# Kernel optimization log

Measured on AMD Instinct MI355X. Metric: run time of the kernel, lower is better.

Reference implementation:

```python
import math
import jax, jax.numpy as jnp
import numpy as np

N, L, D, H = 2, 2048, 1024, 16
DK = D // H  # 64


def setup_inputs() -> dict:
    key = jax.random.key(0)
    k1, k2, k3, k4, k5 = jax.random.split(key, 5)
    scale = 1.0 / math.sqrt(D)
    return {
        "values": jax.random.normal(k1, (N, L, D), dtype=jnp.float32),
        "keys": jax.random.normal(k2, (N, L, D), dtype=jnp.float32),
        "queries": jax.random.normal(k3, (N, L, D), dtype=jnp.float32),
        "fc_out_w": jax.random.normal(k4, (D, D), dtype=jnp.float32) * scale,
        "fc_out_b": jax.random.normal(k5, (D,), dtype=jnp.float32) * scale,
    }


def reference(values, keys, queries, fc_out_w, fc_out_b):
    n, q_len, _ = queries.shape
    k_len = keys.shape[1]
    v = values.reshape(n, k_len, H, DK)
    k = keys.reshape(n, k_len, H, DK)
    q = queries.reshape(n, q_len, H, DK)
    # NOTE: the original module never applies its per-head Linear layers (dead code),
    # and scales logits AFTER the QK einsum.
    energy = jnp.einsum('nqhd,nkhd->nhqk', q, k)  # [N,H,q,k]
    p_attn = jax.nn.softmax(energy / math.sqrt(DK), axis=3)
    attn = jnp.einsum('nhqk,nkhd->nqhd', p_attn, v).reshape(n, q_len, H * DK)
    # fc_out: torch Linear -> x @ W.T + b
    return attn @ fc_out_w.T + fc_out_b
```

## Files before the change

kernel.cpp:

```cpp
#include <hip/hip_runtime.h>
#include <hip/hip_bf16.h>

#define NBATCH 2
#define SEQ    2048
#define DMODEL 1024
#define NHEAD  16
#define DHEAD  64
#define NHTOT  (NBATCH*NHEAD)

typedef __attribute__((ext_vector_type(8)))  short          short8;
typedef __attribute__((ext_vector_type(4)))  float          f32x4;
typedef __attribute__((ext_vector_type(16))) float          f32x16;
typedef __attribute__((ext_vector_type(4)))  unsigned short ushort4v;

__device__ __forceinline__ unsigned short f2bf(float x) {
  union { __hip_bfloat16 b; unsigned short u; } c;
  c.b = __float2bfloat16(x);
  return c.u;
}

__device__ __forceinline__ unsigned int cvt_pk_bf16(float lo, float hi) {
  unsigned int r;
  asm("v_cvt_pk_bf16_f32 %0, %1, %2" : "=v"(r) : "v"(lo), "v"(hi));
  return r;
}

__device__ __forceinline__ void gl_lds16(const unsigned short* g, unsigned short* l) {
  __builtin_amdgcn_global_load_lds(
      (const __attribute__((address_space(1))) void*)g,
      (__attribute__((address_space(3))) void*)l, 16, 0, 0);
}

__global__ __launch_bounds__(256) void cvt_qk(const float* __restrict__ q,
                                              const float* __restrict__ k,
                                              unsigned short* __restrict__ qb,
                                              unsigned short* __restrict__ kb) {
  const float QSCALE = 0.125f * 1.44269504088896340736f;
  int e = (blockIdx.x * 256 + threadIdx.x) * 8;
  int n = e >> 21;
  int r = e & ((1 << 21) - 1);
  int l = r >> 10;
  int c = r & 1023;
  int h = c >> 6;
  int d = c & 63;
  size_t dst = ((size_t)(n * NHEAD + h) * SEQ + l) * DHEAD + d;
  float4 q0 = *reinterpret_cast<const float4*>(q + e);
  float4 q1 = *reinterpret_cast<const float4*>(q + e + 4);
  float4 k0 = *reinterpret_cast<const float4*>(k + e);
  float4 k1 = *reinterpret_cast<const float4*>(k + e + 4);
  union { unsigned short u[8]; short8 s; } qo, ko;
  qo.u[0]=f2bf(q0.x*QSCALE); qo.u[1]=f2bf(q0.y*QSCALE);
  qo.u[2]=f2bf(q0.z*QSCALE); qo.u[3]=f2bf(q0.w*QSCALE);
  qo.u[4]=f2bf(q1.x*QSCALE); qo.u[5]=f2bf(q1.y*QSCALE);
  qo.u[6]=f2bf(q1.z*QSCALE); qo.u[7]=f2bf(q1.w*QSCALE);
  ko.u[0]=f2bf(k0.x); ko.u[1]=f2bf(k0.y); ko.u[2]=f2bf(k0.z); ko.u[3]=f2bf(k0.w);
  ko.u[4]=f2bf(k1.x); ko.u[5]=f2bf(k1.y); ko.u[6]=f2bf(k1.z); ko.u[7]=f2bf(k1.w);
  *reinterpret_cast<short8*>(qb + dst) = qo.s;
  *reinterpret_cast<short8*>(kb + dst) = ko.s;
}

__global__ __launch_bounds__(256) void vtrans(const float* __restrict__ v,
                                              unsigned short* __restrict__ vt) {
  __shared__ __align__(16) unsigned short t[64][76];
  int bid = blockIdx.x;
  int nh = bid >> 5;
  int lt = bid & 31;
  int n = nh >> 4, h = nh & 15;
  int lbase = lt * 64;
  #pragma unroll
  for (int p = 0; p < 4; ++p) {
    int idx = p * 256 + threadIdx.x;
    int e = idx * 4;
    int l = e >> 6, d = e & 63;
    float4 x = *reinterpret_cast<const float4*>(
        v + ((size_t)n * SEQ + lbase + l) * DMODEL + h * DHEAD + d);
    ushort4v o;
    o.x = f2bf(x.x); o.y = f2bf(x.y); o.z = f2bf(x.z); o.w = f2bf(x.w);
    *reinterpret_cast<ushort4v*>(&t[l][d]) = o;
  }
  __syncthreads();
  #pragma unroll
  for (int p = 0; p < 4; ++p) {
    int idx = p * 256 + threadIdx.x;
    int d = idx >> 4, lq = (idx & 15) * 4;
    ushort4v o;
    o.x = t[lq + 0][d]; o.y = t[lq + 1][d];
    o.z = t[lq + 2][d]; o.w = t[lq + 3][d];
    *reinterpret_cast<ushort4v*>(
        vt + ((size_t)nh * DHEAD + d) * SEQ + lbase + lq) = o;
  }
}

__global__ __launch_bounds__(256) void cvt_w(const float* __restrict__ w,
                                             unsigned short* __restrict__ wb) {
  int e = (blockIdx.x * 256 + threadIdx.x) * 8;
  float4 w0 = *reinterpret_cast<const float4*>(w + e);
  float4 w1 = *reinterpret_cast<const float4*>(w + e + 4);
  union { unsigned short u[8]; short8 s; } wo;
  wo.u[0]=f2bf(w0.x); wo.u[1]=f2bf(w0.y); wo.u[2]=f2bf(w0.z); wo.u[3]=f2bf(w0.w);
  wo.u[4]=f2bf(w1.x); wo.u[5]=f2bf(w1.y); wo.u[6]=f2bf(w1.z); wo.u[7]=f2bf(w1.w);
  *reinterpret_cast<short8*>(wb + e) = wo.s;
}

__global__ __launch_bounds__(256, 2) void attn_fwd(const unsigned short* __restrict__ Qb,
                                                   const unsigned short* __restrict__ Kb,
                                                   const unsigned short* __restrict__ Vt,
                                                   unsigned short* __restrict__ Ab) {
  __shared__ __align__(16) unsigned short smem[4 * 4096];

  const int bid = blockIdx.x;
  const int nh = (bid & 7) * 4 + (bid >> 7);
  const int qt = (bid >> 3) & 15;
  const int tid  = threadIdx.x;
  const int wave = tid >> 6;
  const int lane = tid & 63;
  const int l31  = lane & 31;
  const int hi   = lane >> 5;

  const unsigned short* Kb_nh = Kb + (size_t)nh * SEQ * DHEAD;
  const unsigned short* Vt_nh = Vt + (size_t)nh * DHEAD * SEQ;

  const int qglob = qt * 128 + wave * 32 + l31;

  short8 bq[4];
  {
    const unsigned short* Qrow = Qb + ((size_t)nh * SEQ + qglob) * DHEAD + hi * 8;
    #pragma unroll
    for (int ds = 0; ds < 4; ++ds)
      bq[ds] = *reinterpret_cast<const short8*>(Qrow + ds * 16);
  }

  float m_run = -1e30f, l_run = 0.f;
  f32x16 acc[2];
  #pragma unroll
  for (int dt = 0; dt < 2; ++dt)
    #pragma unroll
    for (int r = 0; r < 16; ++r) acc[dt][r] = 0.f;

  int4 kreg[2], vreg[2];
  auto stage_load = [&](int kk) {
    #pragma unroll
    for (int j = 0; j < 2; ++j) {
      int c = j * 256 + tid;
      int row = c >> 3, cs = c & 7;
      kreg[j] = *reinterpret_cast<const int4*>(Kb_nh + (size_t)(kk + row) * DHEAD + cs * 8);
      vreg[j] = *reinterpret_cast<const int4*>(Vt_nh + (size_t)row * SEQ + kk + cs * 8);
    }
  };
  auto stage_write = [&](int buf) {
    unsigned short* kd = smem + buf * 4096;
    unsigned short* vd = smem + 2 * 4096 + buf * 4096;
    #pragma unroll
    for (int j = 0; j < 2; ++j) {
      int c = j * 256 + tid;
      int row = c >> 3, cs = c & 7;
      int dc = cs ^ (row & 7);
      *reinterpret_cast<int4*>(kd + (row * 8 + dc) * 8) = kreg[j];
      *reinterpret_cast<int4*>(vd + (row * 8 + dc) * 8) = vreg[j];
    }
  };

  stage_load(0);
  stage_write(0);
  __syncthreads();

  const int NT = SEQ / 64;
  for (int it = 0; it < NT; ++it) {
    const int cur = it & 1;
    const bool pf = (it + 1 < NT);
    if (pf) stage_load((it + 1) * 64);

    const unsigned short* kb = smem + cur * 4096;
    const unsigned short* vb = smem + 2 * 4096 + cur * 4096;

    f32x16 s[2];
    __builtin_amdgcn_s_setprio(1);
    #pragma unroll
    for (int kt = 0; kt < 2; ++kt) {
      #pragma unroll
      for (int r = 0; r < 16; ++r) s[kt][r] = 0.f;
      const int row = kt * 32 + l31;
      const int sw  = row & 7;
      const unsigned short* kr = kb + row * 64;
      #pragma unroll
      for (int ds = 0; ds < 4; ++ds) {
        short8 ak = *reinterpret_cast<const short8*>(kr + (((ds * 2 + hi) ^ sw) * 8));
        s[kt] = __builtin_amdgcn_mfma_f32_32x32x16_bf16(ak, bq[ds], s[kt], 0, 0, 0);
      }
    }
    __builtin_amdgcn_s_setprio(0);

    float pmax = s[0][0];
    #pragma unroll
    for (int kt = 0; kt < 2; ++kt)
      #pragma unroll
      for (int r = 0; r < 16; ++r) pmax = fmaxf(pmax, s[kt][r]);
    pmax = fmaxf(pmax, __shfl_xor(pmax, 32));

    if (!__all(pmax - m_run <= 8.0f)) {
      float mnew = fmaxf(m_run, pmax);
      float corr = exp2f(m_run - mnew);
      l_run *= corr;
      #pragma unroll
      for (int dt = 0; dt < 2; ++dt)
        #pragma unroll
        for (int r = 0; r < 16; ++r) acc[dt][r] *= corr;
      m_run = mnew;
    }

    float sum = 0.f;
    #pragma unroll
    for (int kt = 0; kt < 2; ++kt)
      #pragma unroll
      for (int r = 0; r < 16; ++r) {
        float p = exp2f(s[kt][r] - m_run);
        s[kt][r] = p;
        sum += p;
      }
    sum += __shfl_xor(sum, 32);
    l_run += sum;

    unsigned int pk[2][8];
    #pragma unroll
    for (int kt = 0; kt < 2; ++kt)
      #pragma unroll
      for (int i = 0; i < 8; ++i)
        pk[kt][i] = cvt_pk_bf16(s[kt][2 * i], s[kt][2 * i + 1]);

    unsigned int pa[4][4];
    #pragma unroll
    for (int ks = 0; ks < 4; ++ks) {
      const int t = ks >> 1, b = (ks & 1) * 4;
      pa[ks][0] = pk[t][b + 0]; pa[ks][2] = pk[t][b + 2];
      asm("v_permlane32_swap_b32 %0, %1" : "+v"(pa[ks][0]), "+v"(pa[ks][2]));
      pa[ks][1] = pk[t][b + 1]; pa[ks][3] = pk[t][b + 3];
      asm("v_permlane32_swap_b32 %0, %1" : "+v"(pa[ks][1]), "+v"(pa[ks][3]));
    }

    if (pf) stage_write(cur ^ 1);

    __builtin_amdgcn_s_setprio(1);
    #pragma unroll
    for (int dt = 0; dt < 2; ++dt) {
      const int row = dt * 32 + l31;
      const int sw  = row & 7;
      const unsigned short* vr = vb + row * 64;
      #pragma unroll
      for (int ks = 0; ks < 4; ++ks) {
        short8 av = *reinterpret_cast<const short8*>(vr + (((ks * 2 + hi) ^ sw) * 8));
        union { unsigned int u[4]; short8 s8; } pu;
        pu.u[0] = pa[ks][0]; pu.u[1] = pa[ks][1];
        pu.u[2] = pa[ks][2]; pu.u[3] = pa[ks][3];
        acc[dt] = __builtin_amdgcn_mfma_f32_32x32x16_bf16(av, pu.s8, acc[dt], 0, 0, 0);
      }
    }
    __builtin_amdgcn_s_setprio(0);
    __syncthreads();
  }

  unsigned short (*obuf)[32][76] = (unsigned short(*)[32][76])(&smem[0]);
  const float inv = 1.0f / l_run;
  const int n = nh >> 4, h = nh & 15;
  #pragma unroll
  for (int dt = 0; dt < 2; ++dt)
    #pragma unroll
    for (int q4 = 0; q4 < 4; ++q4) {
      ushort4v pv;
      pv.x = f2bf(acc[dt][q4 * 4 + 0] * inv);
      pv.y = f2bf(acc[dt][q4 * 4 + 1] * inv);
      pv.z = f2bf(acc[dt][q4 * 4 + 2] * inv);
      pv.w = f2bf(acc[dt][q4 * 4 + 3] * inv);
      *reinterpret_cast<ushort4v*>(&obuf[wave][l31][dt * 32 + q4 * 8 + hi * 4]) = pv;
    }
  __syncthreads();
  #pragma unroll
  for (int rep = 0; rep < 4; ++rep) {
    int idx = rep * 256 + tid;
    int qi = idx >> 3, ch = idx & 7;
    int w = qi >> 5, qr = qi & 31;
    union { unsigned short u[8]; short8 s; } vv;
    #pragma unroll
    for (int i = 0; i < 8; ++i) vv.u[i] = obuf[w][qr][ch * 8 + i];
    size_t orow = (size_t)n * SEQ + qt * 128 + qi;
    *reinterpret_cast<short8*>(Ab + orow * DMODEL + h * 64 + ch * 8) = vv.s;
  }
}

__global__ __launch_bounds__(256, 4) void fc_gemm(const unsigned short* __restrict__ Ab,
                                                  const unsigned short* __restrict__ Wb,
                                                  const float* __restrict__ bias,
                                                  float* __restrict__ out) {
  __shared__ __align__(16) unsigned short At[2][64 * 64];
  __shared__ __align__(16) unsigned short Bt[2][64 * 64];
  const int bid = blockIdx.x;
  const int bn = (bid & 7) * 2 + ((bid >> 3) & 1);
  const int bm = bid >> 4;
  const int tid = threadIdx.x;
  const int wave = tid >> 6, lane = tid & 63;
  const int wr = wave >> 1, wc = wave & 1;
  const int l15 = lane & 15, l4 = lane >> 4;

  f32x4 acc[2][2];
  #pragma unroll
  for (int i = 0; i < 2; ++i)
    #pragma unroll
    for (int j = 0; j < 2; ++j) acc[i][j] = (f32x4){0.f, 0.f, 0.f, 0.f};

  auto stage = [&](int buf, int k0) {
    #pragma unroll
    for (int j = 0; j < 2; ++j) {
      int c = j * 256 + tid;
      int row = c >> 3, cs = c & 7;
      int cg = cs ^ (row & 7);
      int cb = j * 256 + (tid & 192);
      gl_lds16(Ab + (size_t)(bm * 64 + row) * DMODEL + k0 + cg * 8, &At[buf][cb * 8]);
      gl_lds16(Wb + (size_t)(bn * 64 + row) * DMODEL + k0 + cg * 8, &Bt[buf][cb * 8]);
    }
  };

  stage(0, 0);
  __syncthreads();

  const int NT = DMODEL / 64;
  for (int it = 0; it < NT; ++it) {
    int cur = it & 1;
    if (it + 1 < NT) stage(cur ^ 1, (it + 1) * 64);

    #pragma unroll
    for (int s = 0; s < 2; ++s) {
      short8 af[2], bf2[2];
      #pragma unroll
      for (int mt = 0; mt < 2; ++mt) {
        int row = wr * 32 + mt * 16 + l15;
        af[mt] = *reinterpret_cast<const short8*>(
            &At[cur][row * 64 + (((s * 4 + l4) ^ (row & 7)) * 8)]);
      }
      #pragma unroll
      for (int nt = 0; nt < 2; ++nt) {
        int row = wc * 32 + nt * 16 + l15;
        bf2[nt] = *reinterpret_cast<const short8*>(
            &Bt[cur][row * 64 + (((s * 4 + l4) ^ (row & 7)) * 8)]);
      }
      #pragma unroll
      for (int mt = 0; mt < 2; ++mt)
        #pragma unroll
        for (int nt = 0; nt < 2; ++nt)
          acc[mt][nt] = __builtin_amdgcn_mfma_f32_16x16x32_bf16(af[mt], bf2[nt], acc[mt][nt], 0, 0, 0);
    }
    __syncthreads();
  }

  #pragma unroll
  for (int mt = 0; mt < 2; ++mt)
    #pragma unroll
    for (int nt = 0; nt < 2; ++nt) {
      int col = bn * 64 + wc * 32 + nt * 16 + l15;
      float bv = bias[col];
      #pragma unroll
      for (int r = 0; r < 4; ++r) {
        int row = bm * 64 + wr * 32 + mt * 16 + l4 * 4 + r;
        out[(size_t)row * DMODEL + col] = acc[mt][nt][r] + bv;
      }
    }
}

extern "C" void kernel_launch(void* const* d_in, const int* in_sizes, int n_in,
                              void* d_out, int out_size, void* d_ws, size_t ws_size,
                              hipStream_t stream) {
  const float* values  = (const float*)d_in[0];
  const float* keys    = (const float*)d_in[1];
  const float* queries = (const float*)d_in[2];
  const float* fc_w    = (const float*)d_in[3];
  const float* fc_b    = (const float*)d_in[4];
  float* out = (float*)d_out;

  char* ws = (char*)d_ws;
  const size_t QKV_BYTES = (size_t)NHTOT * SEQ * DHEAD * 2;
  unsigned short* Qb = (unsigned short*)(ws);
  unsigned short* Kb = (unsigned short*)(ws + QKV_BYTES);
  unsigned short* Vt = (unsigned short*)(ws + 2 * QKV_BYTES);
  unsigned short* Wb = (unsigned short*)(ws + 3 * QKV_BYTES);
  unsigned short* Ab = (unsigned short*)(ws + 3 * QKV_BYTES + (size_t)DMODEL * DMODEL * 2);

  cvt_qk<<<2048, 256, 0, stream>>>(queries, keys, Qb, Kb);
  vtrans<<<1024, 256, 0, stream>>>(values, Vt);
  cvt_w<<<512, 256, 0, stream>>>(fc_w, Wb);
  attn_fwd<<<NHTOT * (SEQ / 128), 256, 0, stream>>>(Qb, Kb, Vt, Ab);
  fc_gemm<<<(NBATCH * SEQ / 64) * (DMODEL / 64), 256, 0, stream>>>(Ab, Wb, fc_b, out);
}
```

Before: 206.5 us.

## Triple-buffer direct-to-LDS K/V loads in attention and FC GEMM, 512-thread attention blocks

The attention kernel moves to 512-thread blocks covering 256 queries, so each K/V tile staged in LDS is shared by twice as many waves. Register-staged loads become direct global-to-LDS loads into a three-deep ring buffer, with one vmcnt wait and barrier per iteration in place of two syncthreads. The row max and sum reductions become tree reductions, and the output staging uses vector LDS reads. The FC GEMM gets the same three-stage ring with vmcnt waits and setprio, trading extra LDS (lower occupancy bound) and fewer attention blocks (256) for fewer stalls and fewer redundant global loads.

```diff
diff --git a/kernel.cpp b/kernel.cpp
--- a/kernel.cpp
+++ b/kernel.cpp
@@ -102,15 +102,15 @@
   *reinterpret_cast<short8*>(wb + e) = wo.s;
 }
 
-__global__ __launch_bounds__(256, 2) void attn_fwd(const unsigned short* __restrict__ Qb,
+__global__ __launch_bounds__(512, 2) void attn_fwd(const unsigned short* __restrict__ Qb,
                                                    const unsigned short* __restrict__ Kb,
                                                    const unsigned short* __restrict__ Vt,
                                                    unsigned short* __restrict__ Ab) {
-  __shared__ __align__(16) unsigned short smem[4 * 4096];
+  __shared__ __align__(16) unsigned short smem[3 * 8192];
 
   const int bid = blockIdx.x;
-  const int nh = (bid & 7) * 4 + (bid >> 7);
-  const int qt = (bid >> 3) & 15;
+  const int nh = (bid & 7) * 4 + (bid >> 6);
+  const int qt = (bid >> 3) & 7;
   const int tid  = threadIdx.x;
   const int wave = tid >> 6;
   const int lane = tid & 63;
@@ -120,7 +120,7 @@
   const unsigned short* Kb_nh = Kb + (size_t)nh * SEQ * DHEAD;
   const unsigned short* Vt_nh = Vt + (size_t)nh * DHEAD * SEQ;
 
-  const int qglob = qt * 128 + wave * 32 + l31;
+  const int qglob = qt * 256 + wave * 32 + l31;
 
   short8 bq[4];
   {
@@ -137,41 +137,28 @@
     #pragma unroll
     for (int r = 0; r < 16; ++r) acc[dt][r] = 0.f;
 
-  int4 kreg[2], vreg[2];
-  auto stage_load = [&](int kk) {
-    #pragma unroll
-    for (int j = 0; j < 2; ++j) {
-      int c = j * 256 + tid;
-      int row = c >> 3, cs = c & 7;
-      kreg[j] = *reinterpret_cast<const int4*>(Kb_nh + (size_t)(kk + row) * DHEAD + cs * 8);
-      vreg[j] = *reinterpret_cast<const int4*>(Vt_nh + (size_t)row * SEQ + kk + cs * 8);
-    }
+  auto stage = [&](int t) {
+    unsigned short* base = smem + (t % 3) * 8192;
+    int kk  = t * 64;
+    int row = tid >> 3, cs = tid & 7;
+    int cg  = cs ^ (row & 7);
+    int cb  = tid & 448;
+    gl_lds16(Kb_nh + (size_t)(kk + row) * DHEAD + cg * 8, base + cb * 8);
+    gl_lds16(Vt_nh + (size_t)row * SEQ + kk + cg * 8,     base + 4096 + cb * 8);
   };
-  auto stage_write = [&](int buf) {
-    unsigned short* kd = smem + buf * 4096;
-    unsigned short* vd = smem + 2 * 4096 + buf * 4096;
-    #pragma unroll
-    for (int j = 0; j < 2; ++j) {
-      int c = j * 256 + tid;
-      int row = c >> 3, cs = c & 7;
-      int dc = cs ^ (row & 7);
-      *reinterpret_cast<int4*>(kd + (row * 8 + dc) * 8) = kreg[j];
-      *reinterpret_cast<int4*>(vd + (row * 8 + dc) * 8) = vreg[j];
-    }
-  };
-
-  stage_load(0);
-  stage_write(0);
-  __syncthreads();
 
   const int NT = SEQ / 64;
+  stage(0);
+  stage(1);
+
   for (int it = 0; it < NT; ++it) {
-    const int cur = it & 1;
-    const bool pf = (it + 1 < NT);
-    if (pf) stage_load((it + 1) * 64);
-
-    const unsigned short* kb = smem + cur * 4096;
-    const unsigned short* vb = smem + 2 * 4096 + cur * 4096;
+    if (it + 1 < NT) asm volatile("s_waitcnt vmcnt(2)" ::: "memory");
+    else             asm volatile("s_waitcnt vmcnt(0)" ::: "memory");
+    __builtin_amdgcn_s_barrier();
+    if (it + 2 < NT) stage(it + 2);
+
+    const unsigned short* kb = smem + (it % 3) * 8192;
+    const unsigned short* vb = kb + 4096;
 
     f32x16 s[2];
     __builtin_amdgcn_s_setprio(1);
@@ -190,12 +177,14 @@
     }
     __builtin_amdgcn_s_setprio(0);
 
-    float pmax = s[0][0];
-    #pragma unroll
-    for (int kt = 0; kt < 2; ++kt)
-      #pragma unroll
-      for (int r = 0; r < 16; ++r) pmax = fmaxf(pmax, s[kt][r]);
-    pmax = fmaxf(pmax, __shfl_xor(pmax, 32));
+    float tr[16];
+    #pragma unroll
+    for (int i = 0; i < 16; ++i) tr[i] = fmaxf(s[0][i], s[1][i]);
+    #pragma unroll
+    for (int st = 8; st >= 1; st >>= 1)
+      #pragma unroll
+      for (int i = 0; i < st; ++i) tr[i] = fmaxf(tr[i], tr[i + st]);
+    float pmax = fmaxf(tr[0], __shfl_xor(tr[0], 32));
 
     if (!__all(pmax - m_run <= 8.0f)) {
       float mnew = fmaxf(m_run, pmax);
@@ -208,17 +197,17 @@
       m_run = mnew;
     }
 
-    float sum = 0.f;
     #pragma unroll
     for (int kt = 0; kt < 2; ++kt)
       #pragma unroll
-      for (int r = 0; r < 16; ++r) {
-        float p = exp2f(s[kt][r] - m_run);
-        s[kt][r] = p;
-        sum += p;
-      }
-    sum += __shfl_xor(sum, 32);
-    l_run += sum;
+      for (int r = 0; r < 16; ++r) s[kt][r] = exp2f(s[kt][r] - m_run);
+    #pragma unroll
+    for (int i = 0; i < 16; ++i) tr[i] = s[0][i] + s[1][i];
+    #pragma unroll
+    for (int st = 8; st >= 1; st >>= 1)
+      #pragma unroll
+      for (int i = 0; i < st; ++i) tr[i] += tr[i + st];
+    l_run += tr[0] + __shfl_xor(tr[0], 32);
 
     unsigned int pk[2][8];
     #pragma unroll
@@ -237,8 +226,6 @@
       asm("v_permlane32_swap_b32 %0, %1" : "+v"(pa[ks][1]), "+v"(pa[ks][3]));
     }
 
-    if (pf) stage_write(cur ^ 1);
-
     __builtin_amdgcn_s_setprio(1);
     #pragma unroll
     for (int dt = 0; dt < 2; ++dt) {
@@ -255,10 +242,11 @@
       }
     }
     __builtin_amdgcn_s_setprio(0);
-    __syncthreads();
-  }
-
-  unsigned short (*obuf)[32][76] = (unsigned short(*)[32][76])(&smem[0]);
+  }
+
+  __syncthreads();
+
+  unsigned short (*obuf)[32][80] = (unsigned short(*)[32][80])(&smem[0]);
   const float inv = 1.0f / l_run;
   const int n = nh >> 4, h = nh & 15;
   #pragma unroll
@@ -275,23 +263,24 @@
   __syncthreads();
   #pragma unroll
   for (int rep = 0; rep < 4; ++rep) {
-    int idx = rep * 256 + tid;
+    int idx = rep * 512 + tid;
     int qi = idx >> 3, ch = idx & 7;
     int w = qi >> 5, qr = qi & 31;
-    union { unsigned short u[8]; short8 s; } vv;
-    #pragma unroll
-    for (int i = 0; i < 8; ++i) vv.u[i] = obuf[w][qr][ch * 8 + i];
-    size_t orow = (size_t)n * SEQ + qt * 128 + qi;
+    ushort4v v0 = *reinterpret_cast<const ushort4v*>(&obuf[w][qr][ch * 8]);
+    ushort4v v1 = *reinterpret_cast<const ushort4v*>(&obuf[w][qr][ch * 8 + 4]);
+    union { ushort4v h[2]; short8 s; } vv;
+    vv.h[0] = v0; vv.h[1] = v1;
+    size_t orow = (size_t)n * SEQ + qt * 256 + qi;
     *reinterpret_cast<short8*>(Ab + orow * DMODEL + h * 64 + ch * 8) = vv.s;
   }
 }
 
-__global__ __launch_bounds__(256, 4) void fc_gemm(const unsigned short* __restrict__ Ab,
+__global__ __launch_bounds__(256, 3) void fc_gemm(const unsigned short* __restrict__ Ab,
                                                   const unsigned short* __restrict__ Wb,
                                                   const float* __restrict__ bias,
                                                   float* __restrict__ out) {
-  __shared__ __align__(16) unsigned short At[2][64 * 64];
-  __shared__ __align__(16) unsigned short Bt[2][64 * 64];
+  __shared__ __align__(16) unsigned short At[3][64 * 64];
+  __shared__ __align__(16) unsigned short Bt[3][64 * 64];
   const int bid = blockIdx.x;
   const int bn = (bid & 7) * 2 + ((bid >> 3) & 1);
   const int bm = bid >> 4;
@@ -306,7 +295,8 @@
     #pragma unroll
     for (int j = 0; j < 2; ++j) acc[i][j] = (f32x4){0.f, 0.f, 0.f, 0.f};
 
-  auto stage = [&](int buf, int k0) {
+  auto stage = [&](int t) {
+    int buf = t % 3, k0 = t * 64;
     #pragma unroll
     for (int j = 0; j < 2; ++j) {
       int c = j * 256 + tid;
@@ -318,14 +308,18 @@
     }
   };
 
-  stage(0, 0);
-  __syncthreads();
-
   const int NT = DMODEL / 64;
+  stage(0);
+  stage(1);
+
   for (int it = 0; it < NT; ++it) {
-    int cur = it & 1;
-    if (it + 1 < NT) stage(cur ^ 1, (it + 1) * 64);
-
+    if (it + 1 < NT) asm volatile("s_waitcnt vmcnt(4)" ::: "memory");
+    else             asm volatile("s_waitcnt vmcnt(0)" ::: "memory");
+    __builtin_amdgcn_s_barrier();
+    if (it + 2 < NT) stage(it + 2);
+    int cur = it % 3;
+
+    __builtin_amdgcn_s_setprio(1);
     #pragma unroll
     for (int s = 0; s < 2; ++s) {
       short8 af[2], bf2[2];
@@ -347,7 +341,7 @@
         for (int nt = 0; nt < 2; ++nt)
           acc[mt][nt] = __builtin_amdgcn_mfma_f32_16x16x32_bf16(af[mt], bf2[nt], acc[mt][nt], 0, 0, 0);
     }
-    __syncthreads();
+    __builtin_amdgcn_s_setprio(0);
   }
 
   #pragma unroll
@@ -385,6 +379,6 @@
   cvt_qk<<<2048, 256, 0, stream>>>(queries, keys, Qb, Kb);
   vtrans<<<1024, 256, 0, stream>>>(values, Vt);
   cvt_w<<<512, 256, 0, stream>>>(fc_w, Wb);
-  attn_fwd<<<NHTOT * (SEQ / 128), 256, 0, stream>>>(Qb, Kb, Vt, Ab);
+  attn_fwd<<<NHTOT * (SEQ / 256), 512, 0, stream>>>(Qb, Kb, Vt, Ab);
   fc_gemm<<<(NBATCH * SEQ / 64) * (DMODEL / 64), 256, 0, stream>>>(Ab, Wb, fc_b, out);
 }
```

New measurement: 186.3 us. 1.11x faster.
